# Kernel optimization log

Measured on AMD Instinct MI355X. Metric: run time of the kernel, lower is better.

The kernel has to match this reference:

```python
import jax, jax.numpy as jnp
import numpy as np

NUM_JOINTS = 24
PARENTS = np.array([-1, 0, 0, 0, 1, 2, 3, 4, 5, 6, 7, 8, 9, 9, 9, 12, 13, 14, 16, 17, 18, 19, 20, 21])
SENSOR_IDX = np.array([0, 4, 5, 15, 18, 19])          # pelvis, knees, head, elbows (6 IMUs)
IGNORED_IDX = np.array([7, 8, 10, 11, 20, 21, 22, 23])  # ankles, feet, wrists, hands
REDUCED_IDX = np.array([1, 2, 3, 6, 9, 12, 13, 14, 16, 17])  # 10 reduced joints
IGNORED_PARENTS = PARENTS[IGNORED_IDX]


def rotation_6d_to_matrix(d6):
    # pytorch3d convention: rows b1, b2, b3
    a1, a2 = d6[..., :3], d6[..., 3:]
    b1 = a1 / jnp.linalg.norm(a1, axis=-1, keepdims=True)
    b2 = a2 - jnp.sum(b1 * a2, axis=-1, keepdims=True) * b1
    b2 = b2 / jnp.linalg.norm(b2, axis=-1, keepdims=True)
    b3 = jnp.cross(b1, b2)
    return jnp.stack([b1, b2, b3], axis=-2)


def matrix_to_quaternion(m):
    m00, m01, m02 = m[..., 0, 0], m[..., 0, 1], m[..., 0, 2]
    m10, m11, m12 = m[..., 1, 0], m[..., 1, 1], m[..., 1, 2]
    m20, m21, m22 = m[..., 2, 0], m[..., 2, 1], m[..., 2, 2]
    q_abs = jnp.sqrt(jnp.maximum(jnp.stack([
        1.0 + m00 + m11 + m22,
        1.0 + m00 - m11 - m22,
        1.0 - m00 + m11 - m22,
        1.0 - m00 - m11 + m22], axis=-1), 0.0))
    quat_by_rijk = jnp.stack([
        jnp.stack([q_abs[..., 0] ** 2, m21 - m12, m02 - m20, m10 - m01], axis=-1),
        jnp.stack([m21 - m12, q_abs[..., 1] ** 2, m10 + m01, m02 + m20], axis=-1),
        jnp.stack([m02 - m20, m10 + m01, q_abs[..., 2] ** 2, m12 + m21], axis=-1),
        jnp.stack([m10 - m01, m20 + m02, m21 + m12, q_abs[..., 3] ** 2], axis=-1),
    ], axis=-2)
    quat_candidates = quat_by_rijk / (2.0 * jnp.maximum(q_abs[..., None], 0.1))
    idx = jnp.argmax(q_abs, axis=-1)
    return jnp.take_along_axis(quat_candidates, idx[..., None, None], axis=-2)[..., 0, :]


def quaternion_to_axis_angle(q):
    norms = jnp.linalg.norm(q[..., 1:], axis=-1, keepdims=True)
    half_angles = jnp.arctan2(norms, q[..., :1])
    angles = 2.0 * half_angles
    small = jnp.abs(angles) < 1e-6
    safe_angles = jnp.where(small, 1.0, angles)
    sin_half_over_angle = jnp.where(small, 0.5 - angles * angles / 48.0,
                                    jnp.sin(half_angles) / safe_angles)
    return q[..., 1:] / sin_half_over_angle


def matrix_to_axis_angle(m):
    return quaternion_to_axis_angle(matrix_to_quaternion(m))


def setup_inputs() -> dict:
    key = jax.random.key(0)
    k1, k2 = jax.random.split(key)
    B, T = 1024, 256
    glb_reduced_6d = jax.random.normal(k1, (B, T, len(REDUCED_IDX), 6), dtype=jnp.float32)
    orientation_6d = jax.random.normal(k2, (B, T, len(SENSOR_IDX), 6), dtype=jnp.float32)
    return {"glb_reduced_6d": glb_reduced_6d, "orientation_6d": orientation_6d}


def reference(glb_reduced_6d, orientation_6d):
    B, T = glb_reduced_6d.shape[:2]
    BT = B * T
    dtype = glb_reduced_6d.dtype
    glb6 = glb_reduced_6d.reshape(BT, len(REDUCED_IDX), 6)
    ori6 = orientation_6d.reshape(BT, len(SENSOR_IDX), 6)

    orientation = rotation_6d_to_matrix(ori6)          # [BT, 6, 3, 3]
    root = orientation[:, 0]                           # [BT, 3, 3]
    reduced_rot = rotation_6d_to_matrix(glb6)          # [BT, 10, 3, 3]

    # _reduced_glb_6d_to_full_glb_mat
    reduced_glb = jnp.einsum('bij,brjk->brik', root, reduced_rot)
    ori_glb = orientation.at[:, 1:].set(jnp.einsum('bij,bsjk->bsik', root, orientation[:, 1:]))
    eye = jnp.eye(3, dtype=dtype)
    full = jnp.broadcast_to(eye, (BT, NUM_JOINTS, 3, 3))
    full = full.at[:, REDUCED_IDX].set(reduced_glb)
    full = full.at[:, SENSOR_IDX].set(ori_glb)
    # torch advanced-index assignment: RHS gathered from pre-update values
    full = full.at[:, IGNORED_IDX].set(full[:, IGNORED_PARENTS])

    # _global2local: local_i = R_parent(i)^T @ R_i (vectorized over static parent gather)
    parent_rot = full[:, PARENTS[1:]]                  # [BT, 23, 3, 3]
    local_rest = jnp.einsum('bjki,bjkl->bjil', parent_rot, full[:, 1:])
    local = jnp.concatenate([full[:, :1], local_rest], axis=1)
    local = local.at[:, IGNORED_IDX].set(eye)

    pose_aa = matrix_to_axis_angle(local)              # [BT, 24, 3]
    return pose_aa.reshape(B, T, NUM_JOINTS, 3)
```

## Files before the change

kernel.cpp:

```cpp
#include <hip/hip_runtime.h>
#include <math.h>


__device__ __forceinline__ void rot6d_v(float2 u0, float2 u1, float2 u2, float M[3][3]) {
    float a1x = u0.x, a1y = u0.y, a1z = u1.x;
    float a2x = u1.y, a2y = u2.x, a2z = u2.y;
    float r1 = __builtin_amdgcn_rsqf(a1x * a1x + a1y * a1y + a1z * a1z);
    float b1x = a1x * r1, b1y = a1y * r1, b1z = a1z * r1;
    float dt = b1x * a2x + b1y * a2y + b1z * a2z;
    float c2x = a2x - dt * b1x, c2y = a2y - dt * b1y, c2z = a2z - dt * b1z;
    float r2 = __builtin_amdgcn_rsqf(c2x * c2x + c2y * c2y + c2z * c2z);
    float b2x = c2x * r2, b2y = c2y * r2, b2z = c2z * r2;
    float b3x = b1y * b2z - b1z * b2y;
    float b3y = b1z * b2x - b1x * b2z;
    float b3z = b1x * b2y - b1y * b2x;
    M[0][0] = b1x; M[0][1] = b1y; M[0][2] = b1z;
    M[1][0] = b2x; M[1][1] = b2y; M[1][2] = b2z;
    M[2][0] = b3x; M[2][1] = b3y; M[2][2] = b3z;
}

__device__ __forceinline__ void matTmul(const float A[3][3], const float B[3][3], float C[3][3]) {
#pragma unroll
    for (int i = 0; i < 3; ++i)
#pragma unroll
        for (int j = 0; j < 3; ++j)
            C[i][j] = A[0][i] * B[0][j] + A[1][i] * B[1][j] + A[2][i] * B[2][j];
}

__device__ __forceinline__ float atan2_pos(float y, float x) {
    float ax = fabsf(x);
    float mx = fmaxf(y, ax);
    float mn = fminf(y, ax);
    float a = mn * __builtin_amdgcn_rcpf(mx);
    float s = a * a;
    float p = -0.0040540580f;
    p = fmaf(p, s, 0.0218612288f);
    p = fmaf(p, s, -0.0559098861f);
    p = fmaf(p, s, 0.0964200441f);
    p = fmaf(p, s, -0.1390853351f);
    p = fmaf(p, s, 0.1994653599f);
    p = fmaf(p, s, -0.3332985605f);
    p = fmaf(p, s, 0.9999993329f);
    float r = p * a;
    r = (y > ax) ? (1.5707963268f - r) : r;
    r = (x < 0.f) ? (3.1415926536f - r) : r;
    return r;
}

__device__ __forceinline__ void mat2aa(const float m[3][3], float* __restrict__ outp) {
    float m00 = m[0][0], m01 = m[0][1], m02 = m[0][2];
    float m10 = m[1][0], m11 = m[1][1], m12 = m[1][2];
    float m20 = m[2][0], m21 = m[2][1], m22 = m[2][2];
    float t0 = fmaxf(1.f + m00 + m11 + m22, 0.f);
    float t1 = fmaxf(1.f + m00 - m11 - m22, 0.f);
    float t2 = fmaxf(1.f - m00 + m11 - m22, 0.f);
    float t3 = fmaxf(1.f - m00 - m11 + m22, 0.f);
    int idx = 0;
    float bt = t0;
    if (t1 > bt) { bt = t1; idx = 1; }
    if (t2 > bt) { bt = t2; idx = 2; }
    if (t3 > bt) { bt = t3; idx = 3; }
    float best = __builtin_amdgcn_sqrtf(bt);
    float s1 = m21 - m12, s2 = m02 - m20, s3 = m10 - m01;
    float p1 = m10 + m01, p2 = m02 + m20, p3 = m12 + m21;
    float w = (idx == 0) ? bt : (idx == 1) ? s1 : (idx == 2) ? s2 : s3;
    float x = (idx == 0) ? s1 : (idx == 1) ? bt : (idx == 2) ? p1 : p2;
    float y = (idx == 0) ? s2 : (idx == 1) ? p1 : (idx == 2) ? bt : p3;
    float z = (idx == 0) ? s3 : (idx == 1) ? p2 : (idx == 2) ? p3 : bt;
    float inv = 0.5f * __builtin_amdgcn_rcpf(fmaxf(best, 0.1f));
    w *= inv; x *= inv; y *= inv; z *= inv;
    float n = __builtin_amdgcn_sqrtf(x * x + y * y + z * z);
    float half = atan2_pos(n, w);
    float angle = 2.f * half;
    float inv_sh = (angle < 1e-6f) ? 2.f : angle * __builtin_amdgcn_rcpf(n);
    outp[0] = x * inv_sh;
    outp[1] = y * inv_sh;
    outp[2] = z * inv_sh;
}

__global__ __launch_bounds__(256) void pose_kernel(const float* __restrict__ glb,
                                                   const float* __restrict__ ori,
                                                   float* __restrict__ out, int BT) {
    int tid = blockIdx.x * 256 + threadIdx.x;
    int e = tid >> 4;
    if (e >= BT) return;
    int l = tid & 15;

    const float* __restrict__ ge = glb + (size_t)e * 60;
    const float* __restrict__ oe = ori + (size_t)e * 36;
    float* __restrict__ oute = out + (size_t)e * 72;

    const unsigned long long OUT3_LO = 0x1B120F0C09060300ULL;
    const unsigned long long OUT3_HI = 0x393633302D2A2724ULL;
    const unsigned long long SRCJ_LO = 0x0403121102010010ULL;
    const unsigned long long SRCJ_HI = 0x1514090813070605ULL;
    const unsigned long long PL_LO   = 0x0603020100000000ULL;
    const unsigned long long PL_HI   = 0x0D0C0A0908070707ULL;
    const unsigned long long IGN3    = 0x45423F3C211E1815ULL;

    int sh = (l & 7) * 8;
    int out3 = (int)(((l < 8 ? OUT3_LO : OUT3_HI) >> sh) & 0xFF);
    int srcj = (int)(((l < 8 ? SRCJ_LO : SRCJ_HI) >> sh) & 0xFF);
    int pl   = (int)(((l < 8 ? PL_LO   : PL_HI)   >> sh) & 0xFF);

    const float* src = (srcj & 0x10) ? (oe + (srcj & 15) * 6) : (ge + (srcj & 15) * 6);
    const float2* s2 = (const float2*)src;
    float2 u0 = s2[0], u1 = s2[1], u2 = s2[2];

    float X[3][3];
    rot6d_v(u0, u1, u2, X);

    float Xp[3][3];
    {
        const float* xf = &X[0][0];
        float* pf = &Xp[0][0];
#pragma unroll
        for (int k = 0; k < 9; ++k) pf[k] = __shfl(xf[k], pl, 16);
    }

    float L[3][3];
    matTmul(Xp, X, L);
#pragma unroll
    for (int i = 0; i < 3; ++i)
#pragma unroll
        for (int j = 0; j < 3; ++j)
            L[i][j] = (l < 4) ? X[i][j] : L[i][j];

    mat2aa(L, oute + out3);

    if (l < 8) {
        int z = (int)((IGN3 >> sh) & 0xFF);
        float* zp = oute + z;
        zp[0] = 0.f; zp[1] = 0.f; zp[2] = 0.f;
    }
}

extern "C" void kernel_launch(void* const* d_in, const int* in_sizes, int n_in,
                              void* d_out, int out_size, void* d_ws, size_t ws_size,
                              hipStream_t stream) {
    const float* glb = (const float*)d_in[0];
    const float* ori = (const float*)d_in[1];
    float* out = (float*)d_out;
    int BT = in_sizes[0] / 60;
    long long threads = (long long)BT * 16;
    int block = 256;
    int grid = (int)((threads + block - 1) / block);
    pose_kernel<<<grid, block, 0, stream>>>(glb, ori, out, BT);
}
```

Measured before the change: 150.9 us.

## Use grid-stride loop with software-prefetched next-element loads

Replaces the one-element-per-16-lane-group launch with a persistent grid of at most 2048 blocks that loops over elements with a grid stride. Each iteration issues the loads for the next element before computing the current one, with a scheduling barrier so the loads are not reordered after the compute, aiming to hide memory latency. Fewer resident waves may cut latency hiding from occupancy, and the loop adds register pressure and address arithmetic.

```diff
diff --git a/kernel.cpp b/kernel.cpp
--- a/kernel.cpp
+++ b/kernel.cpp
@@ -80,15 +80,12 @@
 
 __global__ __launch_bounds__(256) void pose_kernel(const float* __restrict__ glb,
                                                    const float* __restrict__ ori,
-                                                   float* __restrict__ out, int BT) {
+                                                   float* __restrict__ out,
+                                                   int BT, int stride) {
     int tid = blockIdx.x * 256 + threadIdx.x;
-    int e = tid >> 4;
-    if (e >= BT) return;
+    int g = tid >> 4;
+    if (g >= BT) return;
     int l = tid & 15;
-
-    const float* __restrict__ ge = glb + (size_t)e * 60;
-    const float* __restrict__ oe = ori + (size_t)e * 36;
-    float* __restrict__ oute = out + (size_t)e * 72;
 
     const unsigned long long OUT3_LO = 0x1B120F0C09060300ULL;
     const unsigned long long OUT3_HI = 0x393633302D2A2724ULL;
@@ -102,36 +99,57 @@
     int out3 = (int)(((l < 8 ? OUT3_LO : OUT3_HI) >> sh) & 0xFF);
     int srcj = (int)(((l < 8 ? SRCJ_LO : SRCJ_HI) >> sh) & 0xFF);
     int pl   = (int)(((l < 8 ? PL_LO   : PL_HI)   >> sh) & 0xFF);
+    int z    = (int)((IGN3 >> sh) & 0xFF);
 
-    const float* src = (srcj & 0x10) ? (oe + (srcj & 15) * 6) : (ge + (srcj & 15) * 6);
+    int row6 = (srcj & 15) * 6;
+    bool from_ori = (srcj & 0x10) != 0;
+    const float* sb = from_ori ? ori : glb;
+    int per = from_ori ? 36 : 60;
+
+    const float* src = sb + (size_t)g * per + row6;
+    size_t sstep = (size_t)stride * per;
+    float* po = out + (size_t)g * 72;
+    size_t ostep = (size_t)stride * 72;
+
     const float2* s2 = (const float2*)src;
-    float2 u0 = s2[0], u1 = s2[1], u2 = s2[2];
+    float2 cu0 = s2[0], cu1 = s2[1], cu2 = s2[2];
 
-    float X[3][3];
-    rot6d_v(u0, u1, u2, X);
+    for (int e = g; e < BT; e += stride) {
+        bool more = (e + stride) < BT;
+        const float* nsrc = src + (more ? sstep : 0);
+        const float2* n2 = (const float2*)nsrc;
+        float2 nu0 = n2[0], nu1 = n2[1], nu2 = n2[2];
+        __builtin_amdgcn_sched_barrier(0);
 
-    float Xp[3][3];
-    {
-        const float* xf = &X[0][0];
-        float* pf = &Xp[0][0];
+        float X[3][3];
+        rot6d_v(cu0, cu1, cu2, X);
+
+        float Xp[3][3];
+        {
+            const float* xf = &X[0][0];
+            float* pf = &Xp[0][0];
 #pragma unroll
-        for (int k = 0; k < 9; ++k) pf[k] = __shfl(xf[k], pl, 16);
-    }
+            for (int q = 0; q < 9; ++q) pf[q] = __shfl(xf[q], pl, 16);
+        }
 
-    float L[3][3];
-    matTmul(Xp, X, L);
+        float L[3][3];
+        matTmul(Xp, X, L);
 #pragma unroll
-    for (int i = 0; i < 3; ++i)
+        for (int i = 0; i < 3; ++i)
 #pragma unroll
-        for (int j = 0; j < 3; ++j)
-            L[i][j] = (l < 4) ? X[i][j] : L[i][j];
+            for (int j = 0; j < 3; ++j)
+                L[i][j] = (l < 4) ? X[i][j] : L[i][j];
 
-    mat2aa(L, oute + out3);
+        mat2aa(L, po + out3);
 
-    if (l < 8) {
-        int z = (int)((IGN3 >> sh) & 0xFF);
-        float* zp = oute + z;
-        zp[0] = 0.f; zp[1] = 0.f; zp[2] = 0.f;
+        if (l < 8) {
+            float* zp = po + z;
+            zp[0] = 0.f; zp[1] = 0.f; zp[2] = 0.f;
+        }
+
+        src = nsrc;
+        po += ostep;
+        cu0 = nu0; cu1 = nu1; cu2 = nu2;
     }
 }
 
@@ -142,8 +160,10 @@
     const float* ori = (const float*)d_in[1];
     float* out = (float*)d_out;
     int BT = in_sizes[0] / 60;
-    long long threads = (long long)BT * 16;
-    int block = 256;
-    int grid = (int)((threads + block - 1) / block);
-    pose_kernel<<<grid, block, 0, stream>>>(glb, ori, out, BT);
+    long long groups_needed = (long long)BT;
+    int grid = 2048;
+    long long max_grid = (groups_needed * 16 + 255) / 256;
+    if (max_grid < grid) grid = (int)max_grid;
+    int stride = grid * 16;
+    pose_kernel<<<grid, 256, 0, stream>>>(glb, ori, out, BT, stride);
 }
```

After: 158.6 us. +5.1%, slower.
